# Performance work log

Measured on AMD Instinct MI355X. Metric: run time of the kernel, lower is better.

## Reference

```python
import jax, jax.numpy as jnp
import numpy as np

N = 10000      # nodes
E = 160000     # edges
IN = 256       # input feature dim
HID = 128      # hidden per head
H = 4          # heads (all layers)
EMB = 128      # dim_embedding (last-layer out per head)
SLOPE = 0.2    # leaky_relu negative slope in attention


def _gat_layer(h, src, dst, W, al, ar, b, residual, apply_act):
    """DGL-style GATConv (no dropout). h: [N, F_in], W: [F_in, H*D], al/ar/b: [H, D]."""
    n = h.shape[0]
    heads, d = al.shape
    feat = (h @ W).reshape(n, heads, d)                 # [N, H, D]
    el = jnp.sum(feat * al, axis=-1)                    # [N, H]
    er = jnp.sum(feat * ar, axis=-1)                    # [N, H]
    e = jax.nn.leaky_relu(el[src] + er[dst], SLOPE)     # [E, H]
    # edge softmax over incoming edges of dst (numerically stable)
    m = jax.ops.segment_max(e, dst, num_segments=n)
    m = jnp.where(jnp.isfinite(m), m, 0.0)              # empty segments -> 0
    ex = jnp.exp(e - m[dst])
    den = jax.ops.segment_sum(ex, dst, num_segments=n)
    alpha = ex / jnp.maximum(den[dst], 1e-9)            # [E, H]
    rst = jax.ops.segment_sum(alpha[:, :, None] * feat[src], dst, num_segments=n)  # [N, H, D]
    if residual:
        rst = rst + h.reshape(n, heads, d)              # identity residual (dims match)
    rst = rst + b
    return jax.nn.elu(rst) if apply_act else rst


def setup_inputs() -> dict:
    key = jax.random.key(0)
    ks = jax.random.split(key, 24)
    def p(k, shape, scale):
        return (jax.random.normal(k, shape, jnp.float32) * scale)
    inp = {
        'x': jax.random.normal(ks[0], (N, IN), jnp.float32),
        'src': jax.random.randint(ks[1], (E,), 0, N, dtype=jnp.int32).astype(jnp.int64),
        'dst': jax.random.randint(ks[2], (E,), 0, N, dtype=jnp.int32).astype(jnp.int64),
        # layer 0: in=IN, out=HID per head
        'W0': p(ks[3], (IN, H * HID), 1.0 / np.sqrt(IN)),
        'al0': p(ks[4], (H, HID), 0.1), 'ar0': p(ks[5], (H, HID), 0.1),
        'b0': p(ks[6], (H, HID), 0.02),
        # layer 1: in=H*HID=512, out=HID per head, residual
        'W1': p(ks[7], (H * HID, H * HID), 1.0 / np.sqrt(H * HID)),
        'al1': p(ks[8], (H, HID), 0.1), 'ar1': p(ks[9], (H, HID), 0.1),
        'b1': p(ks[10], (H, HID), 0.02),
        # layer 2: in=H*HID=512, out=EMB per head, residual, no activation
        'W2': p(ks[11], (H * HID, H * EMB), 1.0 / np.sqrt(H * HID)),
        'al2': p(ks[12], (H, EMB), 0.1), 'ar2': p(ks[13], (H, EMB), 0.1),
        'b2': p(ks[14], (H, EMB), 0.02),
        # MLP predictor: 2*EMB -> EMB -> EMB//2 -> 1
        'Wm0': p(ks[15], (2 * EMB, EMB), 1.0 / np.sqrt(2 * EMB)), 'bm0': p(ks[16], (EMB,), 0.02),
        'Wm1': p(ks[17], (EMB, EMB // 2), 1.0 / np.sqrt(EMB)), 'bm1': p(ks[18], (EMB // 2,), 0.02),
        'Wm2': p(ks[19], (EMB // 2, 1), 1.0 / np.sqrt(EMB // 2)), 'bm2': p(ks[20], (1,), 0.02),
    }
    return inp


def reference(x, src, dst, W0, al0, ar0, b0, W1, al1, ar1, b1, W2, al2, ar2, b2,
              Wm0, bm0, Wm1, bm1, Wm2, bm2):
    # GAT encoder
    h = _gat_layer(x, src, dst, W0, al0, ar0, b0, residual=False, apply_act=True).reshape(N, -1)
    h = _gat_layer(h, src, dst, W1, al1, ar1, b1, residual=True, apply_act=True).reshape(N, -1)
    h = _gat_layer(h, src, dst, W2, al2, ar2, b2, residual=True, apply_act=False).mean(axis=1)  # [N, EMB]
    # link predictor over all graph edges
    emb = jnp.concatenate([h[src], h[dst]], axis=1)     # [E, 2*EMB]
    z = jax.nn.relu(emb @ Wm0 + bm0)
    z = jax.nn.relu(z @ Wm1 + bm1)
    return jax.nn.sigmoid(z @ Wm2 + bm2)                # [E, 1]
```

## Files before the change

### kernel.cpp

```cpp
#include <hip/hip_runtime.h>
#include <hip/hip_bf16.h>
#include <math.h>

constexpr int kN = 10000;
constexpr int kE = 160000;
constexpr float kSlope = 0.2f;

typedef short v8s __attribute__((ext_vector_type(8)));
typedef float f32x4 __attribute__((ext_vector_type(4)));
typedef unsigned short ushort_t;

__device__ __forceinline__ float lrelu(float x) { return x > 0.f ? x : kSlope * x; }
__device__ __forceinline__ float elu_f(float x) { return x > 0.f ? x : (expf(x) - 1.f); }
__device__ __forceinline__ float b2f(ushort_t u) {
    return __uint_as_float(((unsigned)u) << 16);
}
__device__ __forceinline__ ushort_t f2b(float f) {
    unsigned u = __float_as_uint(f);
    return (ushort_t)((u + 0x7FFFu + ((u >> 16) & 1u)) >> 16);
}

__global__ void detect_zero(const void* __restrict__ x, const void* __restrict__ dsti,
                            int* __restrict__ flags, int* __restrict__ deg) {
    if (blockIdx.x == 0) {
        __shared__ int sb[2];
        int tid = threadIdx.x;
        if (tid == 0) { sb[0] = 0; sb[1] = 0; }
        __syncthreads();
        const ushort_t* xb = (const ushort_t*)x;
        int big = 0;
        for (int i = tid; i < 4096; i += 256) {
            float v = b2f(xb[i]);
            if (!(fabsf(v) <= 1e4f)) big = 1;
        }
        const int* d32 = (const int*)dsti;
        int hi = 0;
        for (int i = tid; i < 4096; i += 256) hi |= d32[2 * i + 1];
        if (big) atomicOr(&sb[0], 1);
        if (hi)  atomicOr(&sb[1], 1);
        __syncthreads();
        if (tid == 0) { flags[0] = sb[0]; flags[1] = sb[1] ? 0 : 1; }
    } else {
        int i = (blockIdx.x - 1) * 256 + threadIdx.x;
        if (i < 2 * kN) deg[i] = 0;
    }
}

struct PrepArgs {
    const void* sm[13];
    const void* W0; const void* W1; const void* W2; const void* Wm0; const void* Wm1;
    const void* X; const void* srcIn; const void* dstIn;
    float* smallb;
    ushort_t* W0T; ushort_t* W1T; ushort_t* W2T; ushort_t* PQT; ushort_t* Wm1T;
    ushort_t* Xb;
    int* nsrc; int* ndst; int* deg;
    const int* flags;
};
constexpr int kPrepTotal = 4865 + 131072 + 262144 + 262144 + 32768 + 8192 + 2560000 + 320000;

__global__ void prep_all(PrepArgs a) {
    int i = blockIdx.x * 256 + threadIdx.x;
    if (i >= kPrepTotal) return;
    const int f32in = a.flags[0];
    auto cv = [&](const void* p, int idx) -> ushort_t {
        return f32in ? f2b(((const float*)p)[idx]) : ((const ushort_t*)p)[idx];
    };
    if (i < 4865) {
        int seg, offi;
        if (i < 4608)      { seg = i >> 9; offi = i & 511; }
        else if (i < 4736) { seg = 9;  offi = i - 4608; }
        else if (i < 4800) { seg = 10; offi = i - 4736; }
        else if (i < 4864) { seg = 11; offi = i - 4800; }
        else               { seg = 12; offi = 0; }
        a.smallb[i] = f32in ? ((const float*)a.sm[seg])[offi]
                            : b2f(((const ushort_t*)a.sm[seg])[offi]);
        return;
    }
    i -= 4865;
    if (i < 131072) {
        int n = i >> 8, k = i & 255;
        a.W0T[i] = cv(a.W0, k * 512 + n);
        return;
    }
    i -= 131072;
    if (i < 262144) {
        int n = i >> 9, k = i & 511;
        a.W1T[i] = cv(a.W1, k * 512 + n);
        return;
    }
    i -= 262144;
    if (i < 262144) {
        int n = i >> 9, k = i & 511;
        a.W2T[i] = cv(a.W2, k * 512 + n);
        return;
    }
    i -= 262144;
    if (i < 32768) {
        int n = i >> 7, k = i & 127;
        a.PQT[i] = cv(a.Wm0, (k + ((n < 128) ? 0 : 128)) * 128 + (n & 127));
        return;
    }
    i -= 32768;
    if (i < 8192) {
        int n = i >> 7, k = i & 127;
        a.Wm1T[i] = cv(a.Wm1, k * 64 + n);
        return;
    }
    i -= 8192;
    if (i < 2560000) {
        a.Xb[i] = cv(a.X, i);
        return;
    }
    i -= 2560000;
    {
        const void* in = (i < kE) ? a.srcIn : a.dstIn;
        int j = (i < kE) ? i : i - kE;
        int v = a.flags[1] ? (int)((const long long*)in)[j] : ((const int*)in)[j];
        v = ((unsigned)v < (unsigned)kN) ? v : 0;
        if (i < kE) a.nsrc[j] = v;
        else { a.ndst[j] = v; atomicAdd(&a.deg[v], 1); }
    }
}

__global__ __launch_bounds__(1024) void scan_off(const int* __restrict__ deg,
                                                 int* __restrict__ off, int n) {
    __shared__ int s[1024];
    int tid = threadIdx.x;
    int per = (n + 1023) >> 10;
    int base = tid * per;
    int sum = 0;
    for (int i = 0; i < per; ++i) { int j = base + i; if (j < n) sum += deg[j]; }
    s[tid] = sum;
    __syncthreads();
    for (int d = 1; d < 1024; d <<= 1) {
        int v = (tid >= d) ? s[tid - d] : 0;
        __syncthreads();
        s[tid] += v;
        __syncthreads();
    }
    int run = (tid > 0) ? s[tid - 1] : 0;
    for (int i = 0; i < per; ++i) {
        int j = base + i;
        if (j < n) { off[j] = run; run += deg[j]; }
    }
    if (tid == 0) off[n] = s[1023];
}

__global__ void fill_csr(const int* __restrict__ src, const int* __restrict__ dst,
                         const int* __restrict__ off, int* __restrict__ cnt,
                         int* __restrict__ ss, int* __restrict__ eid,
                         int* __restrict__ dpos, int n) {
    int i = blockIdx.x * 256 + threadIdx.x;
    if (i < n) {
        int d = dst[i];
        int pos = off[d] + atomicAdd(&cnt[d], 1);
        if (pos < kE) { ss[pos] = src[i]; eid[pos] = i; dpos[pos] = d; }
    }
}

template <bool ELER>
__global__ __launch_bounds__(256) void gemm_mfma(const ushort_t* __restrict__ A,
                                                 const ushort_t* __restrict__ WT,
                                                 ushort_t* __restrict__ Cout,
                                                 int M, int N, int K,
                                                 const float* __restrict__ al,
                                                 const float* __restrict__ ar,
                                                 float* __restrict__ el,
                                                 float* __restrict__ er) {
    __shared__ __align__(16) ushort_t As[4][64][8];
    __shared__ __align__(16) ushort_t Bs[4][128][8];
    __shared__ float elred[64][2][2];
    const int t = threadIdx.x;
    const int wave = t >> 6, lane = t & 63;
    const int l16 = lane & 15, q = lane >> 4;
    const int row0 = blockIdx.y * 64, col0 = blockIdx.x * 128;
    const int wm = (wave & 1) * 32, wn = (wave >> 1) * 64;
    const int am = t >> 2, ak8 = t & 3;
    const int sw = ak8 * 4;

    const ushort_t* aptr = A + (size_t)min(row0 + am, M - 1) * K + ak8 * 8;
    const ushort_t* bptr0 = WT + (size_t)(col0 + am) * K + ak8 * 8;
    const ushort_t* bptr1 = bptr0 + (size_t)64 * K;

    uint4 ga  = *(const uint4*)aptr;
    uint4 gb0 = *(const uint4*)bptr0;
    uint4 gb1 = *(const uint4*)bptr1;

    f32x4 acc[2][4];
#pragma unroll
    for (int mt = 0; mt < 2; ++mt)
#pragma unroll
        for (int nt = 0; nt < 4; ++nt)
#pragma unroll
            for (int r = 0; r < 4; ++r) acc[mt][nt][r] = 0.f;

    for (int k0 = 0; k0 < K; k0 += 32) {
        __syncthreads();
        *(uint4*)&As[ak8][am ^ sw][0] = ga;
        *(uint4*)&Bs[ak8][am ^ sw][0] = gb0;
        *(uint4*)&Bs[ak8][(am + 64) ^ sw][0] = gb1;
        __syncthreads();
        if (k0 + 32 < K) {
            ga  = *(const uint4*)(aptr + k0 + 32);
            gb0 = *(const uint4*)(bptr0 + k0 + 32);
            gb1 = *(const uint4*)(bptr1 + k0 + 32);
        }
        v8s af[2], bf[4];
        const int qs = q * 4;
#pragma unroll
        for (int mt = 0; mt < 2; ++mt)
            af[mt] = *(const v8s*)&As[q][(wm + mt * 16 + l16) ^ qs][0];
#pragma unroll
        for (int nt = 0; nt < 4; ++nt)
            bf[nt] = *(const v8s*)&Bs[q][(wn + nt * 16 + l16) ^ qs][0];
#pragma unroll
        for (int mt = 0; mt < 2; ++mt)
#pragma unroll
            for (int nt = 0; nt < 4; ++nt)
                acc[mt][nt] = __builtin_amdgcn_mfma_f32_16x16x32_bf16(af[mt], bf[nt],
                                                                      acc[mt][nt], 0, 0, 0);
    }
#pragma unroll
    for (int mt = 0; mt < 2; ++mt)
#pragma unroll
        for (int r = 0; r < 4; ++r) {
            int row = row0 + wm + mt * 16 + q * 4 + r;
            if (row < M) {
#pragma unroll
                for (int nt = 0; nt < 4; ++nt)
                    Cout[(size_t)row * N + col0 + wn + nt * 16 + l16] = f2b(acc[mt][nt][r]);
            }
        }
    if (ELER) {
        const int head = blockIdx.x;
        float alv[4], arv[4];
#pragma unroll
        for (int nt = 0; nt < 4; ++nt) {
            alv[nt] = al[head * 128 + wn + nt * 16 + l16];
            arv[nt] = ar[head * 128 + wn + nt * 16 + l16];
        }
#pragma unroll
        for (int mt = 0; mt < 2; ++mt)
#pragma unroll
            for (int r = 0; r < 4; ++r) {
                float pel = 0.f, per = 0.f;
#pragma unroll
                for (int nt = 0; nt < 4; ++nt) {
                    pel += acc[mt][nt][r] * alv[nt];
                    per += acc[mt][nt][r] * arv[nt];
                }
                pel += __shfl_xor(pel, 1); per += __shfl_xor(per, 1);
                pel += __shfl_xor(pel, 2); per += __shfl_xor(per, 2);
                pel += __shfl_xor(pel, 4); per += __shfl_xor(per, 4);
                pel += __shfl_xor(pel, 8); per += __shfl_xor(per, 8);
                if (l16 == 0) {
                    int rl = wm + mt * 16 + q * 4 + r;
                    elred[rl][wave >> 1][0] = pel;
                    elred[rl][wave >> 1][1] = per;
                }
            }
        __syncthreads();
        if (t < 64) {
            int row = row0 + t;
            if (row < M) {
                el[row * 4 + head] = elred[t][0][0] + elred[t][1][0];
                er[row * 4 + head] = elred[t][0][1] + elred[t][1][1];
            }
        }
    }
}

template <bool RES, bool ACT, int EPI>
__global__ __launch_bounds__(256) void gat_agg(const ushort_t* __restrict__ feat,
                                               const float* __restrict__ el,
                                               const float* __restrict__ er,
                                               const int* __restrict__ off,
                                               const int* __restrict__ ss,
                                               const ushort_t* residb,
                                               const float* __restrict__ bias,
                                               ushort_t* hl) {
    const int node = blockIdx.x * 4 + (threadIdx.x >> 6);
    const int lane = threadIdx.x & 63;
    if (node >= kN) return;
    const int off0 = off[node];
    const int deg = off[node + 1] - off0;
    float4 er4 = *(const float4*)(er + node * 4);
    const int head = lane >> 4;
    const float erh = (head == 0) ? er4.x : (head == 1) ? er4.y : (head == 2) ? er4.z : er4.w;

    const int c0 = lane * 8;
    float den = 0.f;
    float acc[8] = {};
    int s_cur = (deg > 0) ? ss[off0] : 0;
    for (int j = 0; j < deg; ++j) {
        int s_nxt = (j + 1 < deg) ? ss[off0 + j + 1] : 0;
        float e = el[s_cur * 4 + head];
        float wgt = expf(lrelu(e + erh));
        den += wgt;
        const ushort_t* fp = feat + (size_t)s_cur * 512 + c0;
        ushort4 u0 = *(const ushort4*)fp;
        ushort4 u1 = *(const ushort4*)(fp + 4);
        acc[0] += wgt * b2f(u0.x); acc[1] += wgt * b2f(u0.y);
        acc[2] += wgt * b2f(u0.z); acc[3] += wgt * b2f(u0.w);
        acc[4] += wgt * b2f(u1.x); acc[5] += wgt * b2f(u1.y);
        acc[6] += wgt * b2f(u1.z); acc[7] += wgt * b2f(u1.w);
        s_cur = s_nxt;
    }
    const float inv = 1.f / fmaxf(den, 1e-9f);
    float4 b0 = *(const float4*)(bias + c0);
    float4 b1 = *(const float4*)(bias + c0 + 4);
    float v[8] = {acc[0] * inv + b0.x, acc[1] * inv + b0.y,
                  acc[2] * inv + b0.z, acc[3] * inv + b0.w,
                  acc[4] * inv + b1.x, acc[5] * inv + b1.y,
                  acc[6] * inv + b1.z, acc[7] * inv + b1.w};
    if (RES) {
        const ushort_t* rp = residb + (size_t)node * 512 + c0;
        ushort4 r0 = *(const ushort4*)rp;
        ushort4 r1 = *(const ushort4*)(rp + 4);
        v[0] += b2f(r0.x); v[1] += b2f(r0.y); v[2] += b2f(r0.z); v[3] += b2f(r0.w);
        v[4] += b2f(r1.x); v[5] += b2f(r1.y); v[6] += b2f(r1.z); v[7] += b2f(r1.w);
    }
    if (ACT) {
#pragma unroll
        for (int r = 0; r < 8; ++r) v[r] = elu_f(v[r]);
    }
    if (EPI == 1) {
        ushort_t* hp = hl + (size_t)node * 512 + c0;
        ushort4 h0 = {f2b(v[0]), f2b(v[1]), f2b(v[2]), f2b(v[3])};
        ushort4 h1 = {f2b(v[4]), f2b(v[5]), f2b(v[6]), f2b(v[7])};
        *(ushort4*)hp = h0;
        *(ushort4*)(hp + 4) = h1;
    }
    if (EPI == 2) {
        float m[8];
#pragma unroll
        for (int r = 0; r < 8; ++r) {
            float x = v[r] + __shfl_xor(v[r], 16);
            x += __shfl_xor(x, 32);
            m[r] = 0.25f * x;
        }
        if (lane < 16) {
            ushort_t* hp = hl + (size_t)node * 128 + lane * 8;
            ushort4 h0 = {f2b(m[0]), f2b(m[1]), f2b(m[2]), f2b(m[3])};
            ushort4 h1 = {f2b(m[4]), f2b(m[5]), f2b(m[6]), f2b(m[7])};
            *(ushort4*)hp = h0;
            *(ushort4*)(hp + 4) = h1;
        }
    }
}

__global__ __launch_bounds__(256) void edge_mfma(const ushort_t* __restrict__ PQb,
                                                 const float* __restrict__ bm0f,
                                                 const ushort_t* __restrict__ Wm1T,
                                                 const float* __restrict__ bm1f,
                                                 const float* __restrict__ wm2f,
                                                 const float* __restrict__ bm2f,
                                                 const int* __restrict__ ss,
                                                 const int* __restrict__ dpos,
                                                 const int* __restrict__ eid,
                                                 void* __restrict__ outv,
                                                 const int* __restrict__ flags) {
    __shared__ __align__(16) ushort_t zs[64][136];
    const int t = threadIdx.x;
    const int p0 = blockIdx.x * 64;
    const int c4 = (t & 31) * 4;
    float4 bb = *(const float4*)(bm0f + c4);
#pragma unroll
    for (int rep = 0; rep < 8; ++rep) {
        int e_l = rep * 8 + (t >> 5);
        int pos = p0 + e_l;
        int s = ss[pos], d = dpos[pos];
        ushort4 pv = *(const ushort4*)(PQb + (size_t)s * 256 + c4);
        ushort4 qv = *(const ushort4*)(PQb + (size_t)d * 256 + 128 + c4);
        ushort4 hi;
        hi.x = f2b(fmaxf(b2f(pv.x) + b2f(qv.x) + bb.x, 0.f));
        hi.y = f2b(fmaxf(b2f(pv.y) + b2f(qv.y) + bb.y, 0.f));
        hi.z = f2b(fmaxf(b2f(pv.z) + b2f(qv.z) + bb.z, 0.f));
        hi.w = f2b(fmaxf(b2f(pv.w) + b2f(qv.w) + bb.w, 0.f));
        *(ushort4*)&zs[e_l][c4] = hi;
    }
    __syncthreads();

    const int wave = t >> 6, lane = t & 63;
    const int l16 = lane & 15, q = lane >> 4;
    const int ew0 = wave * 16;
    f32x4 acc[4];
#pragma unroll
    for (int nt = 0; nt < 4; ++nt)
#pragma unroll
        for (int r = 0; r < 4; ++r) acc[nt][r] = 0.f;

#pragma unroll
    for (int ks = 0; ks < 4; ++ks) {
        int kq = ks * 32 + q * 8;
        v8s a = *(const v8s*)&zs[ew0 + l16][kq];
#pragma unroll
        for (int nt = 0; nt < 4; ++nt) {
            v8s b = *(const v8s*)(Wm1T + (size_t)(nt * 16 + l16) * 128 + kq);
            acc[nt] = __builtin_amdgcn_mfma_f32_16x16x32_bf16(a, b, acc[nt], 0, 0, 0);
        }
    }
    float b1v[4], w2v[4];
#pragma unroll
    for (int nt = 0; nt < 4; ++nt) {
        b1v[nt] = bm1f[nt * 16 + l16];
        w2v[nt] = wm2f[nt * 16 + l16];
    }
    float b2 = bm2f[0];
    const int f32out = flags[0];
#pragma unroll
    for (int r = 0; r < 4; ++r) {
        float v = 0.f;
#pragma unroll
        for (int nt = 0; nt < 4; ++nt)
            v += fmaxf(acc[nt][r] + b1v[nt], 0.f) * w2v[nt];
        v += __shfl_xor(v, 1);
        v += __shfl_xor(v, 2);
        v += __shfl_xor(v, 4);
        v += __shfl_xor(v, 8);
        if (l16 == 0) {
            int e = eid[p0 + ew0 + q * 4 + r];
            float rr = 1.f / (1.f + expf(-(v + b2)));
            if (f32out) ((float*)outv)[e] = rr;
            else        ((ushort_t*)outv)[e] = f2b(rr);
        }
    }
}

extern "C" void kernel_launch(void* const* d_in, const int* in_sizes, int n_in,
                              void* d_out, int out_size, void* d_ws, size_t ws_size,
                              hipStream_t stream) {
    (void)in_sizes; (void)n_in; (void)out_size; (void)ws_size;

    float* w = (float*)d_ws;
    size_t o = 0;
    auto alloc = [&](size_t n) { float* p = w + o; o += (n + 3) & ~size_t(3); return p; };
    float* smallb = alloc(4868);
    float* al0f = smallb + 0;    float* ar0f = smallb + 512;  float* b0f  = smallb + 1024;
    float* al1f = smallb + 1536; float* ar1f = smallb + 2048; float* b1f  = smallb + 2560;
    float* al2f = smallb + 3072; float* ar2f = smallb + 3584; float* b2f_ = smallb + 4096;
    float* bm0f = smallb + 4608; float* bm1f = smallb + 4736;
    float* wm2f = smallb + 4800; float* bm2f = smallb + 4864;
    float* elb  = alloc((size_t)kN * 4);
    float* erb  = alloc((size_t)kN * 4);
    ushort_t* Fb  = (ushort_t*)alloc((size_t)kN * 256);
    ushort_t* AHL = (ushort_t*)alloc((size_t)kN * 256);
    ushort_t* MHb = (ushort_t*)alloc((size_t)kN * 64);
    ushort_t* Xb  = (ushort_t*)alloc((size_t)kN * 128);
    ushort_t* W0T  = (ushort_t*)alloc(65536);
    ushort_t* W1T  = (ushort_t*)alloc(131072);
    ushort_t* W2T  = (ushort_t*)alloc(131072);
    ushort_t* PQT  = (ushort_t*)alloc(16384);
    ushort_t* Wm1T = (ushort_t*)alloc(4096);
    int* ip    = (int*)(w + o);
    int* flags = ip;
    int* deg   = ip + 4;
    int* cnt   = deg + kN;
    int* off   = cnt + kN;
    int* ss    = off + 10004;
    int* eid   = ss + kE;
    int* dpos  = eid + kE;
    int* nsrc  = dpos + kE;
    int* ndst  = nsrc + kE;

    ushort_t* PQb = Fb;

    dim3 blk(256);

    detect_zero<<<dim3(1 + (2 * kN + 255) / 256), blk, 0, stream>>>(d_in[0], d_in[2], flags, deg);

    PrepArgs a;
    const int sidx[13] = {4, 5, 6, 8, 9, 10, 12, 13, 14, 16, 18, 19, 20};
    for (int i = 0; i < 13; ++i) a.sm[i] = d_in[sidx[i]];
    a.W0 = d_in[3]; a.W1 = d_in[7]; a.W2 = d_in[11]; a.Wm0 = d_in[15]; a.Wm1 = d_in[17];
    a.X = d_in[0]; a.srcIn = d_in[1]; a.dstIn = d_in[2];
    a.smallb = smallb; a.W0T = W0T; a.W1T = W1T; a.W2T = W2T; a.PQT = PQT; a.Wm1T = Wm1T;
    a.Xb = Xb; a.nsrc = nsrc; a.ndst = ndst; a.deg = deg; a.flags = flags;
    prep_all<<<dim3((kPrepTotal + 255) / 256), blk, 0, stream>>>(a);

    scan_off<<<dim3(1), dim3(1024), 0, stream>>>(deg, off, kN);
    fill_csr<<<dim3((kE + 255) / 256), blk, 0, stream>>>(nsrc, ndst, off, cnt, ss, eid, dpos, kE);

    const int gy = (kN + 63) / 64;
    const int ga = (kN + 3) / 4;

    gemm_mfma<true><<<dim3(4, gy), blk, 0, stream>>>(Xb, W0T, Fb, kN, 512, 256,
                                                     al0f, ar0f, elb, erb);
    gat_agg<false, true, 1><<<dim3(ga), blk, 0, stream>>>(Fb, elb, erb, off, ss,
                                                          nullptr, b0f, AHL);

    gemm_mfma<true><<<dim3(4, gy), blk, 0, stream>>>(AHL, W1T, Fb, kN, 512, 512,
                                                     al1f, ar1f, elb, erb);
    gat_agg<true, true, 1><<<dim3(ga), blk, 0, stream>>>(Fb, elb, erb, off, ss,
                                                         AHL, b1f, AHL);

    gemm_mfma<true><<<dim3(4, gy), blk, 0, stream>>>(AHL, W2T, Fb, kN, 512, 512,
                                                     al2f, ar2f, elb, erb);
    gat_agg<true, false, 2><<<dim3(ga), blk, 0, stream>>>(Fb, elb, erb, off, ss,
                                                          AHL, b2f_, MHb);

    gemm_mfma<false><<<dim3(2, gy), blk, 0, stream>>>(MHb, PQT, PQb, kN, 256, 128,
                                                      nullptr, nullptr, nullptr, nullptr);

    edge_mfma<<<dim3(kE / 64), blk, 0, stream>>>(PQb, bm0f, Wm1T, bm1f, wm2f, bm2f,
                                                 ss, dpos, eid, d_out, flags);
}
```

Baseline: 342.2 us.

## Skip bf16 input copy, prefetch aggregation gathers, drop edge kernel LDS staging

```diff
diff --git a/kernel.cpp b/kernel.cpp
--- a/kernel.cpp
+++ b/kernel.cpp
@@ -108,7 +108,7 @@
     }
     i -= 8192;
     if (i < 2560000) {
-        a.Xb[i] = cv(a.X, i);
+        if (f32in) a.Xb[i] = f2b(((const float*)a.X)[i]);
         return;
     }
     i -= 2560000;
@@ -160,6 +160,8 @@
 
 template <bool ELER>
 __global__ __launch_bounds__(256) void gemm_mfma(const ushort_t* __restrict__ A,
+                                                 const void* __restrict__ Araw,
+                                                 const int* __restrict__ gflags,
                                                  const ushort_t* __restrict__ WT,
                                                  ushort_t* __restrict__ Cout,
                                                  int M, int N, int K,
@@ -178,7 +180,10 @@
     const int am = t >> 2, ak8 = t & 3;
     const int sw = ak8 * 4;
 
-    const ushort_t* aptr = A + (size_t)min(row0 + am, M - 1) * K + ak8 * 8;
+    const ushort_t* Aeff = A;
+    if (Araw != nullptr && gflags[0] == 0) Aeff = (const ushort_t*)Araw;
+
+    const ushort_t* aptr = Aeff + (size_t)min(row0 + am, M - 1) * K + ak8 * 8;
     const ushort_t* bptr0 = WT + (size_t)(col0 + am) * K + ak8 * 8;
     const ushort_t* bptr1 = bptr0 + (size_t)64 * K;
 
@@ -291,20 +296,26 @@
     const int c0 = lane * 8;
     float den = 0.f;
     float acc[8] = {};
-    int s_cur = (deg > 0) ? ss[off0] : 0;
-    for (int j = 0; j < deg; ++j) {
-        int s_nxt = (j + 1 < deg) ? ss[off0 + j + 1] : 0;
-        float e = el[s_cur * 4 + head];
-        float wgt = expf(lrelu(e + erh));
-        den += wgt;
-        const ushort_t* fp = feat + (size_t)s_cur * 512 + c0;
-        ushort4 u0 = *(const ushort4*)fp;
-        ushort4 u1 = *(const ushort4*)(fp + 4);
-        acc[0] += wgt * b2f(u0.x); acc[1] += wgt * b2f(u0.y);
-        acc[2] += wgt * b2f(u0.z); acc[3] += wgt * b2f(u0.w);
-        acc[4] += wgt * b2f(u1.x); acc[5] += wgt * b2f(u1.y);
-        acc[6] += wgt * b2f(u1.z); acc[7] += wgt * b2f(u1.w);
-        s_cur = s_nxt;
+    if (deg > 0) {
+        int s_cur = ss[off0];
+        float e_cur = el[s_cur * 4 + head];
+        const ushort_t* fp0 = feat + (size_t)s_cur * 512 + c0;
+        ushort4 u0 = *(const ushort4*)fp0;
+        ushort4 u1 = *(const ushort4*)(fp0 + 4);
+        for (int j = 0; j < deg; ++j) {
+            int s_nxt = (j + 1 < deg) ? ss[off0 + j + 1] : s_cur;
+            float e_nxt = el[s_nxt * 4 + head];
+            const ushort_t* fpn = feat + (size_t)s_nxt * 512 + c0;
+            ushort4 n0 = *(const ushort4*)fpn;
+            ushort4 n1 = *(const ushort4*)(fpn + 4);
+            float wgt = expf(lrelu(e_cur + erh));
+            den += wgt;
+            acc[0] += wgt * b2f(u0.x); acc[1] += wgt * b2f(u0.y);
+            acc[2] += wgt * b2f(u0.z); acc[3] += wgt * b2f(u0.w);
+            acc[4] += wgt * b2f(u1.x); acc[5] += wgt * b2f(u1.y);
+            acc[6] += wgt * b2f(u1.z); acc[7] += wgt * b2f(u1.w);
+            e_cur = e_nxt; u0 = n0; u1 = n1; s_cur = s_nxt;
+        }
     }
     const float inv = 1.f / fmaxf(den, 1e-9f);
     float4 b0 = *(const float4*)(bias + c0);
@@ -360,30 +371,15 @@
                                                  const int* __restrict__ eid,
                                                  void* __restrict__ outv,
                                                  const int* __restrict__ flags) {
-    __shared__ __align__(16) ushort_t zs[64][136];
     const int t = threadIdx.x;
-    const int p0 = blockIdx.x * 64;
-    const int c4 = (t & 31) * 4;
-    float4 bb = *(const float4*)(bm0f + c4);
-#pragma unroll
-    for (int rep = 0; rep < 8; ++rep) {
-        int e_l = rep * 8 + (t >> 5);
-        int pos = p0 + e_l;
-        int s = ss[pos], d = dpos[pos];
-        ushort4 pv = *(const ushort4*)(PQb + (size_t)s * 256 + c4);
-        ushort4 qv = *(const ushort4*)(PQb + (size_t)d * 256 + 128 + c4);
-        ushort4 hi;
-        hi.x = f2b(fmaxf(b2f(pv.x) + b2f(qv.x) + bb.x, 0.f));
-        hi.y = f2b(fmaxf(b2f(pv.y) + b2f(qv.y) + bb.y, 0.f));
-        hi.z = f2b(fmaxf(b2f(pv.z) + b2f(qv.z) + bb.z, 0.f));
-        hi.w = f2b(fmaxf(b2f(pv.w) + b2f(qv.w) + bb.w, 0.f));
-        *(ushort4*)&zs[e_l][c4] = hi;
-    }
-    __syncthreads();
-
     const int wave = t >> 6, lane = t & 63;
     const int l16 = lane & 15, q = lane >> 4;
-    const int ew0 = wave * 16;
+    const int base = blockIdx.x * 64 + wave * 16;
+    const int pos = base + l16;
+    const int s = ss[pos], d = dpos[pos];
+    const ushort_t* prow = PQb + (size_t)s * 256;
+    const ushort_t* qrow = PQb + (size_t)d * 256 + 128;
+
     f32x4 acc[4];
 #pragma unroll
     for (int nt = 0; nt < 4; ++nt)
@@ -392,11 +388,25 @@
 
 #pragma unroll
     for (int ks = 0; ks < 4; ++ks) {
-        int kq = ks * 32 + q * 8;
-        v8s a = *(const v8s*)&zs[ew0 + l16][kq];
+        const int k0 = ks * 32 + q * 8;
+        ushort4 p0 = *(const ushort4*)(prow + k0);
+        ushort4 p1 = *(const ushort4*)(prow + k0 + 4);
+        ushort4 q0 = *(const ushort4*)(qrow + k0);
+        ushort4 q1 = *(const ushort4*)(qrow + k0 + 4);
+        float4 bb0 = *(const float4*)(bm0f + k0);
+        float4 bb1 = *(const float4*)(bm0f + k0 + 4);
+        v8s a;
+        a[0] = (short)f2b(fmaxf(b2f(p0.x) + b2f(q0.x) + bb0.x, 0.f));
+        a[1] = (short)f2b(fmaxf(b2f(p0.y) + b2f(q0.y) + bb0.y, 0.f));
+        a[2] = (short)f2b(fmaxf(b2f(p0.z) + b2f(q0.z) + bb0.z, 0.f));
+        a[3] = (short)f2b(fmaxf(b2f(p0.w) + b2f(q0.w) + bb0.w, 0.f));
+        a[4] = (short)f2b(fmaxf(b2f(p1.x) + b2f(q1.x) + bb1.x, 0.f));
+        a[5] = (short)f2b(fmaxf(b2f(p1.y) + b2f(q1.y) + bb1.y, 0.f));
+        a[6] = (short)f2b(fmaxf(b2f(p1.z) + b2f(q1.z) + bb1.z, 0.f));
+        a[7] = (short)f2b(fmaxf(b2f(p1.w) + b2f(q1.w) + bb1.w, 0.f));
 #pragma unroll
         for (int nt = 0; nt < 4; ++nt) {
-            v8s b = *(const v8s*)(Wm1T + (size_t)(nt * 16 + l16) * 128 + kq);
+            v8s b = *(const v8s*)(Wm1T + (size_t)(nt * 16 + l16) * 128 + k0);
             acc[nt] = __builtin_amdgcn_mfma_f32_16x16x32_bf16(a, b, acc[nt], 0, 0, 0);
         }
     }
@@ -419,7 +429,7 @@
         v += __shfl_xor(v, 4);
         v += __shfl_xor(v, 8);
         if (l16 == 0) {
-            int e = eid[p0 + ew0 + q * 4 + r];
+            int e = eid[base + q * 4 + r];
             float rr = 1.f / (1.f + expf(-(v + b2)));
             if (f32out) ((float*)outv)[e] = rr;
             else        ((ushort_t*)outv)[e] = f2b(rr);
@@ -484,22 +494,23 @@
     const int gy = (kN + 63) / 64;
     const int ga = (kN + 3) / 4;
 
-    gemm_mfma<true><<<dim3(4, gy), blk, 0, stream>>>(Xb, W0T, Fb, kN, 512, 256,
-                                                     al0f, ar0f, elb, erb);
+    gemm_mfma<true><<<dim3(4, gy), blk, 0, stream>>>(Xb, d_in[0], flags, W0T, Fb,
+                                                     kN, 512, 256, al0f, ar0f, elb, erb);
     gat_agg<false, true, 1><<<dim3(ga), blk, 0, stream>>>(Fb, elb, erb, off, ss,
                                                           nullptr, b0f, AHL);
 
-    gemm_mfma<true><<<dim3(4, gy), blk, 0, stream>>>(AHL, W1T, Fb, kN, 512, 512,
-                                                     al1f, ar1f, elb, erb);
+    gemm_mfma<true><<<dim3(4, gy), blk, 0, stream>>>(AHL, nullptr, flags, W1T, Fb,
+                                                     kN, 512, 512, al1f, ar1f, elb, erb);
     gat_agg<true, true, 1><<<dim3(ga), blk, 0, stream>>>(Fb, elb, erb, off, ss,
                                                          AHL, b1f, AHL);
 
-    gemm_mfma<true><<<dim3(4, gy), blk, 0, stream>>>(AHL, W2T, Fb, kN, 512, 512,
-                                                     al2f, ar2f, elb, erb);
+    gemm_mfma<true><<<dim3(4, gy), blk, 0, stream>>>(AHL, nullptr, flags, W2T, Fb,
+                                                     kN, 512, 512, al2f, ar2f, elb, erb);
     gat_agg<true, false, 2><<<dim3(ga), blk, 0, stream>>>(Fb, elb, erb, off, ss,
                                                           AHL, b2f_, MHb);
 
-    gemm_mfma<false><<<dim3(2, gy), blk, 0, stream>>>(MHb, PQT, PQb, kN, 256, 128,
+    gemm_mfma<false><<<dim3(2, gy), blk, 0, stream>>>(MHb, nullptr, flags, PQT, PQb,
+                                                      kN, 256, 128,
                                                       nullptr, nullptr, nullptr, nullptr);
 
     edge_mfma<<<dim3(kE / 64), blk, 0, stream>>>(PQb, bm0f, Wm1T, bm1f, wm2f, bm2f,
```

New measurement: 331.7 us. -3.1%, faster.
